# Optimization experiments

Measured on AMD Instinct MI355X. Metric: run time of the kernel, lower is better.

Reference implementation:

```python
import jax, jax.numpy as jnp
import numpy as np

B, N_SIDE, S = 64, 40, 512
N = N_SIDE * N_SIDE          # 1600 grid points (fl_feature_dims [1,40,40])
EMB = 10                     # embedding_dim
GDIM = 8                     # lie('homography').dim
WIDTH = 128
C1 = 20                      # first-layer output channels


def _embed(x, emb_dim):
    # sinusoidal embedding of each scalar coordinate: [..., D] -> [..., D*emb_dim]
    freqs = 2.0 ** jnp.arange(emb_dim // 2, dtype=x.dtype)
    ang = x[..., None] * freqs                       # [..., D, emb/2]
    e = jnp.concatenate([jnp.sin(ang), jnp.cos(ang)], axis=-1)  # [..., D, emb]
    return e.reshape(x.shape[:-1] + (x.shape[-1] * emb_dim,))


def _glorot(key, shape):
    fan_in = shape[0]
    return jax.random.normal(key, shape, dtype=jnp.float32) / np.sqrt(fan_in)


def setup_inputs() -> dict:
    key = jax.random.key(0)
    ks = jax.random.split(key, 16)
    inp = {
        'data':   jax.random.normal(ks[0], (B, N, 1), dtype=jnp.float32),
        'v0':     jax.random.normal(ks[1], (S, GDIM), dtype=jnp.float32),
        'v_last': jax.random.normal(ks[2], (S, GDIM), dtype=jnp.float32),
        # FirstLayer filter MLP: 2*EMB -> 20 -> 20 -> 1*C1
        'fl_w1': _glorot(ks[3], (2 * EMB, 20)), 'fl_b1': jnp.zeros((20,), jnp.float32),
        'fl_w2': _glorot(ks[4], (20, 20)),      'fl_b2': jnp.zeros((20,), jnp.float32),
        'fl_w3': _glorot(ks[5], (20, C1)),      'fl_b3': jnp.zeros((C1,), jnp.float32),
        # Hidden FilterMLP: EMB*GDIM=80 -> WIDTH -> C1*WIDTH
        's_w1': _glorot(ks[6], (EMB * GDIM, WIDTH)), 's_b1': jnp.zeros((WIDTH,), jnp.float32),
        's_w2': _glorot(ks[7], (WIDTH, C1 * WIDTH)), 's_b2': jnp.zeros((C1 * WIDTH,), jnp.float32),
        'fc1_w': _glorot(ks[8], (WIDTH, WIDTH)), 'fc1_b': jnp.zeros((WIDTH,), jnp.float32),
        'fc2_w': _glorot(ks[9], (WIDTH, WIDTH)), 'fc2_b': jnp.zeros((WIDTH,), jnp.float32),
        'pool_w': _glorot(ks[10], (WIDTH, 10)),  'pool_b': jnp.zeros((10,), jnp.float32),
    }
    return inp


def reference(data, v0, v_last, fl_w1, fl_b1, fl_w2, fl_b2, fl_w3, fl_b3,
              s_w1, s_b1, s_w2, s_b2, fc1_w, fc1_b, fc2_w, fc2_b, pool_w, pool_b):
    silu = jax.nn.silu
    # pixel grid in [-1,1]^2, homogeneous coords [N,3]
    lin = jnp.linspace(-1.0, 1.0, N_SIDE, dtype=data.dtype)
    xx, yy = jnp.meshgrid(lin, lin, indexing='ij')
    coords = jnp.stack([xx.ravel(), yy.ravel()], axis=-1)           # [N,2]
    xh = jnp.concatenate([coords, jnp.ones((N, 1), data.dtype)], -1)  # [N,3]
    # homography matrices: identity + small perturbation from 8 group params
    pert = jnp.concatenate([0.1 * v_last, jnp.zeros((S, 1), data.dtype)], -1).reshape(S, 3, 3)
    H = jnp.eye(3, dtype=data.dtype) + pert                          # [S,3,3]
    y = jnp.einsum('sij,nj->sni', H, xh)                             # [S,N,3]
    t = y[..., :2] / y[..., 2:3]                                     # projective action [S,N,2]
    # continuous-kernel first layer: filters generated by MLP on embedded coords
    e1 = _embed(t, EMB)                                              # [S,N,20]
    h = silu(e1 @ fl_w1 + fl_b1)
    h = silu(h @ fl_w2 + fl_b2)
    filt1 = h @ fl_w3 + fl_b3                                        # [S,N,C1]
    z = jnp.einsum('bn,sno->bso', data[:, :, 0], filt1) / N          # [B,S,C1]
    z = silu(z)
    # hidden FilterMLP on group samples v0 -> per-sample filters [S,C1,WIDTH]
    v0e = _embed(v0, EMB)                                            # [S,80]
    h2 = silu(v0e @ s_w1 + s_b1)                                     # [S,WIDTH]
    filt2 = (h2 @ s_w2 + s_b2).reshape(S, C1, WIDTH)
    # (1/S) * sum over group-sample and channel axes of broadcast product
    z = jnp.einsum('bsc,scw->bw', z, filt2) / S                      # [B,WIDTH]
    z = silu(z @ fc1_w + fc1_b) + z
    z = silu(z @ fc2_w + fc2_b) + z
    return z @ pool_w + pool_b                                       # [B,10]
```

## Files before the change

kernel.cpp:

```cpp
#include <hip/hip_runtime.h>

#define N_PTS 1600
#define NSIDE 40
#define SNUM  512
#define BNUM  64
#define C1D   20
#define WID   128

typedef _Float16 h8  __attribute__((ext_vector_type(8)));
typedef _Float16 h4  __attribute__((ext_vector_type(4)));
typedef __fp16   h2v __attribute__((ext_vector_type(2)));
typedef float    f4  __attribute__((ext_vector_type(4)));

__device__ __forceinline__ float silu_f(float x){
    return x * __builtin_amdgcn_rcpf(1.f + __expf(-x));
}
__device__ __forceinline__ void fma4(float4& a, float s, const float4 w){
    a.x += s*w.x; a.y += s*w.y; a.z += s*w.z; a.w += s*w.w;
}

__global__ __launch_bounds__(512) void kp_prep(
    const float* __restrict__ data, const float* __restrict__ v0,
    const float* __restrict__ s_w1, const float* __restrict__ s_b1,
    const float* __restrict__ s_w2,
    _Float16* __restrict__ dataA, _Float16* __restrict__ s_w2hT,
    _Float16* __restrict__ h2G, float* __restrict__ out2g)
{
    const int t = threadIdx.x, bx = blockIdx.x;
    if (bx >= 32) {
        if (bx < 112) {
            const int u  = (bx - 32) * 512 + t;
            const int n  = u >> 4, k0 = (u & 15) * 8;
            h8 v;
            #pragma unroll
            for (int j = 0; j < 8; j++) v[j] = (_Float16)s_w2[(k0 + j) * 2560 + n];
            *(h8*)(s_w2hT + n * 128 + k0) = v;
        } else if (bx < 137) {
            const int o  = (bx - 112) * 512 + t;
            const int L  = o & 63, cm = o >> 6;
            const int mt = cm & 3, ch = cm >> 2;
            const int b  = mt * 16 + (L & 15);
            const int nb = ch * 32 + (L >> 4) * 8;
            const float* src = data + b * N_PTS + nb;
            h8 v;
            #pragma unroll
            for (int j = 0; j < 8; j++) v[j] = (_Float16)src[j];
            *(h8*)(dataA + (size_t)o * 8) = v;
        } else {
            for (int v = t; v < 8192; v += 512) out2g[v] = 0.f;
        }
        return;
    }
    const int s0 = bx * 16;
    __shared__ __align__(16) _Float16 w1T[12288];
    __shared__ __align__(16) _Float16 svtA[1536];
    for (int u = t; u < 12288; u += 512) {
        const int j = u / 96, k = u - j * 96;
        w1T[u] = (_Float16)((k < 80) ? s_w1[k * 128 + j] : 0.f);
    }
    for (int u = t; u < 1536; u += 512) svtA[u] = (_Float16)0.f;
    __syncthreads();
    if (t < 128) {
        const int ss = t >> 3, d = t & 7;
        const float val = v0[(s0 + ss) * 8 + d];
        float sv, cv;
        __sincosf(val, &sv, &cv);
        #pragma unroll
        for (int k = 0; k < 5; k++) {
            svtA[ss * 96 + d * 10 + k]     = (_Float16)sv;
            svtA[ss * 96 + d * 10 + 5 + k] = (_Float16)cv;
            const float ns = 2.f * sv * cv, nc = 1.f - 2.f * sv * sv;
            sv = ns; cv = nc;
        }
    }
    __syncthreads();
    const int lane = t & 63, w = t >> 6;
    const int q = lane >> 4, l15 = lane & 15;
    const f4 zero4 = (f4)(0.f);
    f4 D = zero4;
    #pragma unroll
    for (int kc = 0; kc < 3; kc++) {
        const h8 af = *(const h8*)(svtA + l15 * 96 + kc * 32 + q * 8);
        const h8 bf = *(const h8*)(w1T + (w * 16 + l15) * 96 + kc * 32 + q * 8);
        D = __builtin_amdgcn_mfma_f32_16x16x32_f16(af, bf, D, 0, 0, 0);
    }
    const float b = s_b1[w * 16 + l15];
    #pragma unroll
    for (int r = 0; r < 4; r++)
        h2G[(s0 + q * 4 + r) * 128 + w * 16 + l15] = (_Float16)silu_f(D[r] + b);
}

__device__ __forceinline__ void embed_coord(
    int n, float hA, float hB, float hC, float h6, float h7, float h8c,
    h2v e5[5])
{
    const int i = n / NSIDE;
    const int j = n - i * NSIDE;
    const float x = -1.f + (float)i * (2.f/39.f);
    const float y = -1.f + (float)j * (2.f/39.f);
    const float yc = hA*x + hB*y + hC;
    const float y2 = h6*x + h7*y + h8c;
    const float tc = yc * __builtin_amdgcn_rcpf(y2);
    float e[10];
    float sv, cv;
    __sincosf(tc, &sv, &cv);
    #pragma unroll
    for (int k = 0; k < 5; k++) {
        e[k] = sv; e[5+k] = cv;
        const float ns = 2.f*sv*cv, nc = 1.f - 2.f*sv*sv; sv = ns; cv = nc;
    }
    #pragma unroll
    for (int k = 0; k < 5; k++)
        e5[k] = __builtin_amdgcn_cvt_pkrtz(e[2*k], e[2*k+1]);
}

#define ASTRIDE 40

__global__ __launch_bounds__(512, 8) void kaf_fused(
    const float* __restrict__ v_last,
    const float* __restrict__ w1, const float* __restrict__ b1,
    const float* __restrict__ w2, const float* __restrict__ b2,
    const float* __restrict__ w3, const float* __restrict__ b3,
    const float* __restrict__ s_b2,
    const _Float16* __restrict__ s_w2hT, const _Float16* __restrict__ h2G,
    float* __restrict__ f2g, _Float16* __restrict__ filtG)
{
    const int t  = threadIdx.x;
    const int bx = blockIdx.x;
    const int lane = t & 63, w = t >> 6;
    const int q = lane >> 4, l15 = lane & 15;
    const f4 zero4 = (f4)(0.f);

    __shared__ __align__(16) unsigned char smem[27008];

    if (bx >= 1024) {
        const int bxe = bx - 1024;
        const int mt = bxe / 10, ct = bxe - mt * 10;
        h8 af[4];
        #pragma unroll
        for (int kc = 0; kc < 4; kc++)
            af[kc] = *(const h8*)(h2G + (mt * 16 + l15) * 128 + kc * 32 + q * 8);
        #pragma unroll
        for (int i = 0; i < 2; i++) {
            const int n0 = ct * 256 + (w + 8 * i) * 16;
            f4 D = zero4;
            #pragma unroll
            for (int kc = 0; kc < 4; kc++) {
                const h8 bf = *(const h8*)(s_w2hT + (n0 + l15) * 128 + kc * 32 + q * 8);
                D = __builtin_amdgcn_mfma_f32_16x16x32_f16(af[kc], bf, D, 0, 0, 0);
            }
            const float bb = s_b2[n0 + l15];
            #pragma unroll
            for (int r = 0; r < 4; r++)
                f2g[(mt * 16 + q * 4 + r) * 2560 + n0 + l15] = D[r] + bb;
        }
        return;
    }

    const int s    = bx & 511;
    const int half = bx >> 9;
    const int nb0  = half * 800;
    const int ep   = lane >> 1;
    const int ec   = lane & 1;
    const int erow = w*16 + ep + ((ep >> 4) * 112);

    _Float16* act  = (_Float16*)smem;
    _Float16* wlds = (_Float16*)(smem + 20480);
    float*    blds = (float*)   (smem + 26624);

    {
        const float* wsrc[3] = { w1, w2, w3 };
        const float* bsrc[3] = { b1, b2, b3 };
        for (int v = t; v < 3072; v += 512) {
            const int l = v >> 10, rem = v & 1023;
            const int cout = rem >> 5, cin = rem & 31;
            float x = 0.f;
            if (cout < 20 && cin < 20) x = wsrc[l][cin * 20 + cout];
            wlds[v] = (_Float16)x;
        }
        if (t < 96) {
            const int l = t >> 5, cout = t & 31;
            blds[t] = (cout < 20) ? bsrc[l][cout] : 0.f;
        }
    }

    float Hm[9];
    #pragma unroll
    for (int k = 0; k < 9; k++) Hm[k] = (k == 0 || k == 4 || k == 8) ? 1.f : 0.f;
    #pragma unroll
    for (int k = 0; k < 8; k++) Hm[k] += 0.1f * v_last[s*8 + k];
    const float hA = ec ? Hm[3] : Hm[0];
    const float hB = ec ? Hm[4] : Hm[1];
    const float hC = ec ? Hm[5] : Hm[2];

    if (ec == 0) {
        unsigned long long* pz = (unsigned long long*)(act + erow*ASTRIDE + 20);
        pz[0] = 0ull; pz[1] = 0ull; pz[2] = 0ull;
    }

    __syncthreads();

    _Float16* fgs = filtG + (size_t)(half*512 + s) * 16000;

    for (int base = 0; base < 800; base += 256) {
        const int tn = min(256, 800 - base);

        if (erow < tn) {
            h2v e5[5];
            embed_coord(nb0 + base + erow, hA, hB, hC, Hm[6], Hm[7], Hm[8], e5);
            #pragma unroll
            for (int k = 0; k < 5; k++)
                *(h2v*)(act + erow*ASTRIDE + ec*10 + 2*k) = e5[k];
        }

        const int nmt  = tn >> 4;
        const bool hasA = w < nmt;
        const bool hasB = (w + 8) < nmt;
        const int rA = w * 16, rB = (w + 8) * 16;

        #pragma unroll
        for (int l = 0; l < 2; l++) {
            const h8 wf0 = *(const h8*)(wlds + ((l*2+0)*16 + l15) * 32 + q*8);
            const h8 wf1 = *(const h8*)(wlds + ((l*2+1)*16 + l15) * 32 + q*8);
            const float4 bD0 = *(const float4*)&blds[l*32 + q*4];
            const float4 bD1 = *(const float4*)&blds[l*32 + 16 + q*4];
            if (hasA) {
                const h8 af = *(const h8*)(act + (rA + l15)*ASTRIDE + q*8);
                const f4 D0 = __builtin_amdgcn_mfma_f32_16x16x32_f16(wf0, af, zero4, 0, 0, 0);
                const f4 D1 = __builtin_amdgcn_mfma_f32_16x16x32_f16(wf1, af, zero4, 0, 0, 0);
                h4 pv;
                pv[0] = (_Float16)silu_f(D0[0] + bD0.x);
                pv[1] = (_Float16)silu_f(D0[1] + bD0.y);
                pv[2] = (_Float16)silu_f(D0[2] + bD0.z);
                pv[3] = (_Float16)silu_f(D0[3] + bD0.w);
                *(h4*)(act + (rA + l15)*ASTRIDE + q*4) = pv;
                if (q == 0) {
                    h4 pu;
                    pu[0] = (_Float16)silu_f(D1[0] + bD1.x);
                    pu[1] = (_Float16)silu_f(D1[1] + bD1.y);
                    pu[2] = (_Float16)silu_f(D1[2] + bD1.z);
                    pu[3] = (_Float16)silu_f(D1[3] + bD1.w);
                    *(h4*)(act + (rA + l15)*ASTRIDE + 16) = pu;
                }
            }
            if (hasB) {
                const h8 af = *(const h8*)(act + (rB + l15)*ASTRIDE + q*8);
                const f4 D0 = __builtin_amdgcn_mfma_f32_16x16x32_f16(wf0, af, zero4, 0, 0, 0);
                const f4 D1 = __builtin_amdgcn_mfma_f32_16x16x32_f16(wf1, af, zero4, 0, 0, 0);
                h4 pv;
                pv[0] = (_Float16)silu_f(D0[0] + bD0.x);
                pv[1] = (_Float16)silu_f(D0[1] + bD0.y);
                pv[2] = (_Float16)silu_f(D0[2] + bD0.z);
                pv[3] = (_Float16)silu_f(D0[3] + bD0.w);
                *(h4*)(act + (rB + l15)*ASTRIDE + q*4) = pv;
                if (q == 0) {
                    h4 pu;
                    pu[0] = (_Float16)silu_f(D1[0] + bD1.x);
                    pu[1] = (_Float16)silu_f(D1[1] + bD1.y);
                    pu[2] = (_Float16)silu_f(D1[2] + bD1.z);
                    pu[3] = (_Float16)silu_f(D1[3] + bD1.w);
                    *(h4*)(act + (rB + l15)*ASTRIDE + 16) = pu;
                }
            }
        }
        {
            const h8 wf0 = *(const h8*)(wlds + (64 + l15) * 32 + q*8);
            const h8 wf1 = *(const h8*)(wlds + (80 + l15) * 32 + q*8);
            const float b20 = blds[64 + l15];
            const float b21 = blds[80 + l15];
            for (int mt = w; mt < nmt; mt += 8) {
                const int r0 = mt * 16;
                const h8 af = *(const h8*)(act + (r0 + l15)*ASTRIDE + q*8);
                f4 D0 = __builtin_amdgcn_mfma_f32_16x16x32_f16(af, wf0, zero4, 0, 0, 0);
                f4 D1 = __builtin_amdgcn_mfma_f32_16x16x32_f16(af, wf1, zero4, 0, 0, 0);
                h4 p0, p1;
                #pragma unroll
                for (int r = 0; r < 4; r++) {
                    p0[r] = (_Float16)(D0[r] + b20);
                    p1[r] = (_Float16)(D1[r] + b21);
                }
                *(h4*)(fgs + l15*800 + base + r0 + q*4) = p0;
                if (l15 < 4)
                    *(h4*)(fgs + (16 + l15)*800 + base + r0 + q*4) = p1;
            }
        }
    }
}

__global__ __launch_bounds__(256, 6) void kz_gemm(
    const _Float16* __restrict__ dataA, const _Float16* __restrict__ filtG,
    float* __restrict__ zpart)
{
    const int s    = blockIdx.x & 511;
    const int half = blockIdx.x >> 9;
    const int t    = threadIdx.x;
    const int lane = t & 63;
    const int w    = t >> 6;
    const int q    = lane >> 4;
    const int l15  = lane & 15;

    __shared__ __align__(16) float red[4 * 64 * 21];

    const _Float16* fgs = filtG + (size_t)(half*512 + s) * 16000;
    const int r1row = (l15 < 4) ? (16 + l15) : 0;

    f4 zacc[4][2];
    #pragma unroll
    for (int mt = 0; mt < 4; mt++) { zacc[mt][0] = (f4)(0.f); zacc[mt][1] = (f4)(0.f); }

    #pragma unroll 2
    for (int kc = w; kc < 25; kc += 4) {
        const h8 bf0 = *(const h8*)(fgs + l15  *800 + kc*32 + q*8);
        const h8 bf1 = *(const h8*)(fgs + r1row*800 + kc*32 + q*8);
        const int gchunk = half*25 + kc;
        #pragma unroll
        for (int mt = 0; mt < 4; mt++) {
            const h8 afz = *(const h8*)(dataA + ((size_t)(gchunk*4 + mt)*64 + lane)*8);
            zacc[mt][0] = __builtin_amdgcn_mfma_f32_16x16x32_f16(afz, bf0, zacc[mt][0], 0, 0, 0);
            zacc[mt][1] = __builtin_amdgcn_mfma_f32_16x16x32_f16(afz, bf1, zacc[mt][1], 0, 0, 0);
        }
    }

    #pragma unroll
    for (int mt = 0; mt < 4; mt++) {
        #pragma unroll
        for (int r = 0; r < 4; r++) {
            const int b = mt*16 + q*4 + r;
            red[(w*64 + b)*21 + l15] = zacc[mt][0][r];
            if (l15 < 4) red[(w*64 + b)*21 + 16 + l15] = zacc[mt][1][r];
        }
    }
    __syncthreads();
    for (int v = t; v < 1280; v += 256) {
        const int c = v >> 6, b = v & 63;
        const float sum = red[(      b)*21 + c] + red[( 64 + b)*21 + c]
                        + red[(128 + b)*21 + c] + red[(192 + b)*21 + c];
        zpart[(half*512 + s)*1280 + v] = sum;
    }
}

__global__ __launch_bounds__(256) void k2_contract(
    const float* __restrict__ zg, const float* __restrict__ f2g,
    float* __restrict__ out2g)
{
    const int blk = blockIdx.x;
    const int sg  = blk >> 2;
    const int wq  = blk & 3;
    const int s0  = sg * 4;
    const int w0  = wq * 32;
    const int t   = threadIdx.x;
    __shared__ __align__(16) float zl[4*1280];
    __shared__ __align__(16) float fl[4*20*32];
    #pragma unroll
    for (int sp = 0; sp < 4; sp++) {
        const int srow = (s0 + sp) * 1280;
        for (int r = t; r < 1280; r += 256) {
            const float a0 = zg[srow + r];
            const float a1 = zg[512*1280 + srow + r];
            zl[sp*1280 + r] = silu_f((a0 + a1) * (1.f / (float)N_PTS));
        }
        for (int u = t; u < 640; u += 256) {
            const int c = u >> 5, ww = u & 31;
            fl[sp*640 + u] = f2g[(s0 + sp)*2560 + c*128 + w0 + ww];
        }
    }
    __syncthreads();
    const int ww = t & 31, bh = t >> 5;
    float4 acc[2];
    acc[0] = make_float4(0.f, 0.f, 0.f, 0.f);
    acc[1] = make_float4(0.f, 0.f, 0.f, 0.f);
    #pragma unroll 4
    for (int sc = 0; sc < 80; sc++) {
        const float f = fl[sc * 32 + ww];
        const float4* zz = (const float4*)&zl[sc * 64 + bh * 8];
        fma4(acc[0], f, zz[0]);
        fma4(acc[1], f, zz[1]);
    }
    const float* af = (const float*)acc;
    #pragma unroll
    for (int idx = 0; idx < 8; idx++) {
        const int b = bh * 8 + idx;
        atomicAdd(&out2g[b * 128 + w0 + ww], af[idx]);
    }
}

__global__ __launch_bounds__(128) void k3_tail(
    const float* __restrict__ out2g,
    const float* __restrict__ fc1w, const float* __restrict__ fc1b,
    const float* __restrict__ fc2w, const float* __restrict__ fc2b,
    const float* __restrict__ pw,   const float* __restrict__ pb,
    float* __restrict__ out)
{
    const int b = blockIdx.x, t = threadIdx.x;
    __shared__ float zb[128], r1[128], r2[128];
    zb[t] = out2g[b * 128 + t] * (1.f / (float)SNUM);
    __syncthreads();
    float a = fc1b[t];
    #pragma unroll 8
    for (int i = 0; i < 128; i++) a += zb[i] * fc1w[i * 128 + t];
    r1[t] = silu_f(a) + zb[t];
    __syncthreads();
    a = fc2b[t];
    #pragma unroll 8
    for (int i = 0; i < 128; i++) a += r1[i] * fc2w[i * 128 + t];
    r2[t] = silu_f(a) + r1[t];
    __syncthreads();
    if (t < 10) {
        float o = pb[t];
        #pragma unroll 8
        for (int i = 0; i < 128; i++) o += r2[i] * pw[i * 10 + t];
        out[b * 10 + t] = o;
    }
}

extern "C" void kernel_launch(void* const* d_in, const int* in_sizes, int n_in,
                              void* d_out, int out_size, void* d_ws, size_t ws_size,
                              hipStream_t stream) {
    const float* data   = (const float*)d_in[0];
    const float* v0     = (const float*)d_in[1];
    const float* v_last = (const float*)d_in[2];
    const float* fl_w1  = (const float*)d_in[3];
    const float* fl_b1  = (const float*)d_in[4];
    const float* fl_w2  = (const float*)d_in[5];
    const float* fl_b2  = (const float*)d_in[6];
    const float* fl_w3  = (const float*)d_in[7];
    const float* fl_b3  = (const float*)d_in[8];
    const float* s_w1   = (const float*)d_in[9];
    const float* s_b1   = (const float*)d_in[10];
    const float* s_w2   = (const float*)d_in[11];
    const float* s_b2   = (const float*)d_in[12];
    const float* fc1_w  = (const float*)d_in[13];
    const float* fc1_b  = (const float*)d_in[14];
    const float* fc2_w  = (const float*)d_in[15];
    const float* fc2_b  = (const float*)d_in[16];
    const float* pool_w = (const float*)d_in[17];
    const float* pool_b = (const float*)d_in[18];
    float* out = (float*)d_out;

    float* ws        = (float*)d_ws;
    _Float16* dataA  = (_Float16*)ws;
    float* zpart  = ws    + 51200;
    float* f2g    = zpart + 1310720;
    float* out2g  = f2g   + 1310720;
    _Float16* s_w2hT = (_Float16*)(out2g + 8192);
    _Float16* h2G    = (_Float16*)(out2g + 8192 + 163840);
    _Float16* filtG  = (_Float16*)(out2g + 8192 + 163840 + 32768);

    kp_prep    <<<138, 512, 0, stream>>>(data, v0, s_w1, s_b1, s_w2,
                                         dataA, s_w2hT, h2G, out2g);
    kaf_fused  <<<1344, 512, 0, stream>>>(v_last,
                                          fl_w1, fl_b1, fl_w2, fl_b2, fl_w3, fl_b3,
                                          s_b2, s_w2hT, h2G, f2g, filtG);
    kz_gemm    <<<1024, 256, 0, stream>>>(dataA, filtG, zpart);
    k2_contract<<<512, 256, 0, stream>>>(zpart, f2g, out2g);
    k3_tail    <<<64, 128, 0, stream>>>(out2g, fc1_w, fc1_b, fc2_w, fc2_b,
                                        pool_w, pool_b, out);
}
```

Baseline: 164.2 us.

## Fuse filter generation with data contraction, keeping filters in LDS

```diff
diff --git a/kernel.cpp b/kernel.cpp
--- a/kernel.cpp
+++ b/kernel.cpp
@@ -116,14 +116,15 @@
 
 #define ASTRIDE 40
 
-__global__ __launch_bounds__(512, 8) void kaf_fused(
+__global__ __launch_bounds__(512, 8) void kfz_fused(
     const float* __restrict__ v_last,
     const float* __restrict__ w1, const float* __restrict__ b1,
     const float* __restrict__ w2, const float* __restrict__ b2,
     const float* __restrict__ w3, const float* __restrict__ b3,
     const float* __restrict__ s_b2,
     const _Float16* __restrict__ s_w2hT, const _Float16* __restrict__ h2G,
-    float* __restrict__ f2g, _Float16* __restrict__ filtG)
+    const _Float16* __restrict__ dataA,
+    float* __restrict__ f2g, float* __restrict__ zpart)
 {
     const int t  = threadIdx.x;
     const int bx = blockIdx.x;
@@ -131,7 +132,7 @@
     const int q = lane >> 4, l15 = lane & 15;
     const f4 zero4 = (f4)(0.f);
 
-    __shared__ __align__(16) unsigned char smem[27008];
+    __shared__ __align__(16) unsigned char smem[37632];
 
     if (bx >= 1024) {
         const int bxe = bx - 1024;
@@ -163,10 +164,14 @@
     const int ep   = lane >> 1;
     const int ec   = lane & 1;
     const int erow = w*16 + ep + ((ep >> 4) * 112);
-
-    _Float16* act  = (_Float16*)smem;
-    _Float16* wlds = (_Float16*)(smem + 20480);
-    float*    blds = (float*)   (smem + 26624);
+    const int mtbase = (w & 1) * 2;
+    const int kcs    = w >> 1;
+
+    _Float16* act   = (_Float16*)smem;
+    _Float16* filtB = (_Float16*)(smem + 20480);
+    _Float16* wlds  = (_Float16*)(smem + 31040);
+    float*    blds  = (float*)   (smem + 37184);
+    float*    red   = (float*)smem;
 
     {
         const float* wsrc[3] = { w1, w2, w3 };
@@ -198,9 +203,11 @@
         pz[0] = 0ull; pz[1] = 0ull; pz[2] = 0ull;
     }
 
-    __syncthreads();
-
-    _Float16* fgs = filtG + (size_t)(half*512 + s) * 16000;
+    f4 zacc[2][2];
+    #pragma unroll
+    for (int mi = 0; mi < 2; mi++) { zacc[mi][0] = zero4; zacc[mi][1] = zero4; }
+
+    __syncthreads();
 
     for (int base = 0; base < 800; base += 256) {
         const int tn = min(256, 800 - base);
@@ -279,62 +286,51 @@
                     p0[r] = (_Float16)(D0[r] + b20);
                     p1[r] = (_Float16)(D1[r] + b21);
                 }
-                *(h4*)(fgs + l15*800 + base + r0 + q*4) = p0;
+                *(h4*)(filtB + l15*264 + r0 + q*4) = p0;
                 if (l15 < 4)
-                    *(h4*)(fgs + (16 + l15)*800 + base + r0 + q*4) = p1;
+                    *(h4*)(filtB + (16 + l15)*264 + r0 + q*4) = p1;
             }
         }
-    }
-}
-
-__global__ __launch_bounds__(256, 6) void kz_gemm(
-    const _Float16* __restrict__ dataA, const _Float16* __restrict__ filtG,
-    float* __restrict__ zpart)
-{
-    const int s    = blockIdx.x & 511;
-    const int half = blockIdx.x >> 9;
-    const int t    = threadIdx.x;
-    const int lane = t & 63;
-    const int w    = t >> 6;
-    const int q    = lane >> 4;
-    const int l15  = lane & 15;
-
-    __shared__ __align__(16) float red[4 * 64 * 21];
-
-    const _Float16* fgs = filtG + (size_t)(half*512 + s) * 16000;
-    const int r1row = (l15 < 4) ? (16 + l15) : 0;
-
-    f4 zacc[4][2];
-    #pragma unroll
-    for (int mt = 0; mt < 4; mt++) { zacc[mt][0] = (f4)(0.f); zacc[mt][1] = (f4)(0.f); }
-
-    #pragma unroll 2
-    for (int kc = w; kc < 25; kc += 4) {
-        const h8 bf0 = *(const h8*)(fgs + l15  *800 + kc*32 + q*8);
-        const h8 bf1 = *(const h8*)(fgs + r1row*800 + kc*32 + q*8);
-        const int gchunk = half*25 + kc;
-        #pragma unroll
-        for (int mt = 0; mt < 4; mt++) {
-            const h8 afz = *(const h8*)(dataA + ((size_t)(gchunk*4 + mt)*64 + lane)*8);
-            zacc[mt][0] = __builtin_amdgcn_mfma_f32_16x16x32_f16(afz, bf0, zacc[mt][0], 0, 0, 0);
-            zacc[mt][1] = __builtin_amdgcn_mfma_f32_16x16x32_f16(afz, bf1, zacc[mt][1], 0, 0, 0);
-        }
-    }
-
-    #pragma unroll
-    for (int mt = 0; mt < 4; mt++) {
+        __syncthreads();
+
+        const int nkc = tn >> 5;
+        const int r1row = (l15 < 4) ? (16 + l15) : 0;
+        #pragma unroll
+        for (int kk = 0; kk < 2; kk++) {
+            const int kc = kcs + kk*4;
+            if (kc < nkc) {
+                const int gchunk = ((nb0 + base) >> 5) + kc;
+                const h8 bf0 = *(const h8*)(filtB + l15  *264 + kc*32 + q*8);
+                const h8 bf1 = *(const h8*)(filtB + r1row*264 + kc*32 + q*8);
+                #pragma unroll
+                for (int mi = 0; mi < 2; mi++) {
+                    const int mt = mtbase + mi;
+                    const h8 afz = *(const h8*)(dataA + ((size_t)(gchunk*4 + mt)*64 + lane)*8);
+                    zacc[mi][0] = __builtin_amdgcn_mfma_f32_16x16x32_f16(afz, bf0, zacc[mi][0], 0, 0, 0);
+                    zacc[mi][1] = __builtin_amdgcn_mfma_f32_16x16x32_f16(afz, bf1, zacc[mi][1], 0, 0, 0);
+                }
+            }
+        }
+        __syncthreads();
+    }
+
+    #pragma unroll
+    for (int mi = 0; mi < 2; mi++) {
         #pragma unroll
         for (int r = 0; r < 4; r++) {
-            const int b = mt*16 + q*4 + r;
-            red[(w*64 + b)*21 + l15] = zacc[mt][0][r];
-            if (l15 < 4) red[(w*64 + b)*21 + 16 + l15] = zacc[mt][1][r];
-        }
-    }
-    __syncthreads();
-    for (int v = t; v < 1280; v += 256) {
+            const int bl = mi*16 + q*4 + r;
+            red[(w*32 + bl)*21 + l15] = zacc[mi][0][r];
+            if (l15 < 4) red[(w*32 + bl)*21 + 16 + l15] = zacc[mi][1][r];
+        }
+    }
+    __syncthreads();
+    for (int v = t; v < 1280; v += 512) {
         const int c = v >> 6, b = v & 63;
-        const float sum = red[(      b)*21 + c] + red[( 64 + b)*21 + c]
-                        + red[(128 + b)*21 + c] + red[(192 + b)*21 + c];
+        const int mts = b >> 5, bl = b & 31;
+        const float sum = red[((mts    )*32 + bl)*21 + c]
+                        + red[((mts + 2)*32 + bl)*21 + c]
+                        + red[((mts + 4)*32 + bl)*21 + c]
+                        + red[((mts + 6)*32 + bl)*21 + c];
         zpart[(half*512 + s)*1280 + v] = sum;
     }
 }
@@ -444,14 +440,12 @@
     float* out2g  = f2g   + 1310720;
     _Float16* s_w2hT = (_Float16*)(out2g + 8192);
     _Float16* h2G    = (_Float16*)(out2g + 8192 + 163840);
-    _Float16* filtG  = (_Float16*)(out2g + 8192 + 163840 + 32768);
 
     kp_prep    <<<138, 512, 0, stream>>>(data, v0, s_w1, s_b1, s_w2,
                                          dataA, s_w2hT, h2G, out2g);
-    kaf_fused  <<<1344, 512, 0, stream>>>(v_last,
+    kfz_fused  <<<1344, 512, 0, stream>>>(v_last,
                                           fl_w1, fl_b1, fl_w2, fl_b2, fl_w3, fl_b3,
-                                          s_b2, s_w2hT, h2G, f2g, filtG);
-    kz_gemm    <<<1024, 256, 0, stream>>>(dataA, filtG, zpart);
+                                          s_b2, s_w2hT, h2G, dataA, f2g, zpart);
     k2_contract<<<512, 256, 0, stream>>>(zpart, f2g, out2g);
     k3_tail    <<<64, 128, 0, stream>>>(out2g, fc1_w, fc1_b, fc2_w, fc2_b,
                                         pool_w, pool_b, out);
```

New measurement: 167.7 us. +2.2%, slower.

## Replace MFMA tile-based filter MLP with per-thread scalar FP32 MLP

Applied to the files above, without the earlier changes.

```diff
diff --git a/kernel.cpp b/kernel.cpp
--- a/kernel.cpp
+++ b/kernel.cpp
@@ -9,7 +9,6 @@
 
 typedef _Float16 h8  __attribute__((ext_vector_type(8)));
 typedef _Float16 h4  __attribute__((ext_vector_type(4)));
-typedef __fp16   h2v __attribute__((ext_vector_type(2)));
 typedef float    f4  __attribute__((ext_vector_type(4)));
 
 __device__ __forceinline__ float silu_f(float x){
@@ -90,33 +89,7 @@
         h2G[(s0 + q * 4 + r) * 128 + w * 16 + l15] = (_Float16)silu_f(D[r] + b);
 }
 
-__device__ __forceinline__ void embed_coord(
-    int n, float hA, float hB, float hC, float h6, float h7, float h8c,
-    h2v e5[5])
-{
-    const int i = n / NSIDE;
-    const int j = n - i * NSIDE;
-    const float x = -1.f + (float)i * (2.f/39.f);
-    const float y = -1.f + (float)j * (2.f/39.f);
-    const float yc = hA*x + hB*y + hC;
-    const float y2 = h6*x + h7*y + h8c;
-    const float tc = yc * __builtin_amdgcn_rcpf(y2);
-    float e[10];
-    float sv, cv;
-    __sincosf(tc, &sv, &cv);
-    #pragma unroll
-    for (int k = 0; k < 5; k++) {
-        e[k] = sv; e[5+k] = cv;
-        const float ns = 2.f*sv*cv, nc = 1.f - 2.f*sv*sv; sv = ns; cv = nc;
-    }
-    #pragma unroll
-    for (int k = 0; k < 5; k++)
-        e5[k] = __builtin_amdgcn_cvt_pkrtz(e[2*k], e[2*k+1]);
-}
-
-#define ASTRIDE 40
-
-__global__ __launch_bounds__(512, 8) void kaf_fused(
+__global__ __launch_bounds__(512) void kfv_filt(
     const float* __restrict__ v_last,
     const float* __restrict__ w1, const float* __restrict__ b1,
     const float* __restrict__ w2, const float* __restrict__ b2,
@@ -127,14 +100,12 @@
 {
     const int t  = threadIdx.x;
     const int bx = blockIdx.x;
-    const int lane = t & 63, w = t >> 6;
-    const int q = lane >> 4, l15 = lane & 15;
-    const f4 zero4 = (f4)(0.f);
-
-    __shared__ __align__(16) unsigned char smem[27008];
-
-    if (bx >= 1024) {
-        const int bxe = bx - 1024;
+
+    if (bx >= 1600) {
+        const int lane = t & 63, w = t >> 6;
+        const int q = lane >> 4, l15 = lane & 15;
+        const f4 zero4 = (f4)(0.f);
+        const int bxe = bx - 1600;
         const int mt = bxe / 10, ct = bxe - mt * 10;
         h8 af[4];
         #pragma unroll
@@ -157,134 +128,81 @@
         return;
     }
 
-    const int s    = bx & 511;
-    const int half = bx >> 9;
-    const int nb0  = half * 800;
-    const int ep   = lane >> 1;
-    const int ec   = lane & 1;
-    const int erow = w*16 + ep + ((ep >> 4) * 112);
-
-    _Float16* act  = (_Float16*)smem;
-    _Float16* wlds = (_Float16*)(smem + 20480);
-    float*    blds = (float*)   (smem + 26624);
-
+    const int tid  = bx * 512 + t;
+    const int s    = tid / 1600;
+    const int p    = tid - s * 1600;
+    const int half = (p >= 800) ? 1 : 0;
+    const int row  = p - half * 800;
+
+    float Hm[9];
+    #pragma unroll
+    for (int k = 0; k < 9; k++) Hm[k] = (k == 0 || k == 4 || k == 8) ? 1.f : 0.f;
+    #pragma unroll
+    for (int k = 0; k < 8; k++) Hm[k] += 0.1f * v_last[s * 8 + k];
+
+    const int gi = p / NSIDE;
+    const int gj = p - gi * NSIDE;
+    const float x = -1.f + (float)gi * (2.f / 39.f);
+    const float y = -1.f + (float)gj * (2.f / 39.f);
+    const float den = Hm[6] * x + Hm[7] * y + Hm[8];
+    const float inv = __builtin_amdgcn_rcpf(den);
+    const float t0 = (Hm[0] * x + Hm[1] * y + Hm[2]) * inv;
+    const float t1 = (Hm[3] * x + Hm[4] * y + Hm[5]) * inv;
+
+    float e[20];
     {
-        const float* wsrc[3] = { w1, w2, w3 };
-        const float* bsrc[3] = { b1, b2, b3 };
-        for (int v = t; v < 3072; v += 512) {
-            const int l = v >> 10, rem = v & 1023;
-            const int cout = rem >> 5, cin = rem & 31;
-            float x = 0.f;
-            if (cout < 20 && cin < 20) x = wsrc[l][cin * 20 + cout];
-            wlds[v] = (_Float16)x;
-        }
-        if (t < 96) {
-            const int l = t >> 5, cout = t & 31;
-            blds[t] = (cout < 20) ? bsrc[l][cout] : 0.f;
-        }
-    }
-
-    float Hm[9];
-    #pragma unroll
-    for (int k = 0; k < 9; k++) Hm[k] = (k == 0 || k == 4 || k == 8) ? 1.f : 0.f;
-    #pragma unroll
-    for (int k = 0; k < 8; k++) Hm[k] += 0.1f * v_last[s*8 + k];
-    const float hA = ec ? Hm[3] : Hm[0];
-    const float hB = ec ? Hm[4] : Hm[1];
-    const float hC = ec ? Hm[5] : Hm[2];
-
-    if (ec == 0) {
-        unsigned long long* pz = (unsigned long long*)(act + erow*ASTRIDE + 20);
-        pz[0] = 0ull; pz[1] = 0ull; pz[2] = 0ull;
-    }
-
-    __syncthreads();
-
-    _Float16* fgs = filtG + (size_t)(half*512 + s) * 16000;
-
-    for (int base = 0; base < 800; base += 256) {
-        const int tn = min(256, 800 - base);
-
-        if (erow < tn) {
-            h2v e5[5];
-            embed_coord(nb0 + base + erow, hA, hB, hC, Hm[6], Hm[7], Hm[8], e5);
-            #pragma unroll
-            for (int k = 0; k < 5; k++)
-                *(h2v*)(act + erow*ASTRIDE + ec*10 + 2*k) = e5[k];
-        }
-
-        const int nmt  = tn >> 4;
-        const bool hasA = w < nmt;
-        const bool hasB = (w + 8) < nmt;
-        const int rA = w * 16, rB = (w + 8) * 16;
-
-        #pragma unroll
-        for (int l = 0; l < 2; l++) {
-            const h8 wf0 = *(const h8*)(wlds + ((l*2+0)*16 + l15) * 32 + q*8);
-            const h8 wf1 = *(const h8*)(wlds + ((l*2+1)*16 + l15) * 32 + q*8);
-            const float4 bD0 = *(const float4*)&blds[l*32 + q*4];
-            const float4 bD1 = *(const float4*)&blds[l*32 + 16 + q*4];
-            if (hasA) {
-                const h8 af = *(const h8*)(act + (rA + l15)*ASTRIDE + q*8);
-                const f4 D0 = __builtin_amdgcn_mfma_f32_16x16x32_f16(wf0, af, zero4, 0, 0, 0);
-                const f4 D1 = __builtin_amdgcn_mfma_f32_16x16x32_f16(wf1, af, zero4, 0, 0, 0);
-                h4 pv;
-                pv[0] = (_Float16)silu_f(D0[0] + bD0.x);
-                pv[1] = (_Float16)silu_f(D0[1] + bD0.y);
-                pv[2] = (_Float16)silu_f(D0[2] + bD0.z);
-                pv[3] = (_Float16)silu_f(D0[3] + bD0.w);
-                *(h4*)(act + (rA + l15)*ASTRIDE + q*4) = pv;
-                if (q == 0) {
-                    h4 pu;
-                    pu[0] = (_Float16)silu_f(D1[0] + bD1.x);
-                    pu[1] = (_Float16)silu_f(D1[1] + bD1.y);
-                    pu[2] = (_Float16)silu_f(D1[2] + bD1.z);
-                    pu[3] = (_Float16)silu_f(D1[3] + bD1.w);
-                    *(h4*)(act + (rA + l15)*ASTRIDE + 16) = pu;
-                }
-            }
-            if (hasB) {
-                const h8 af = *(const h8*)(act + (rB + l15)*ASTRIDE + q*8);
-                const f4 D0 = __builtin_amdgcn_mfma_f32_16x16x32_f16(wf0, af, zero4, 0, 0, 0);
-                const f4 D1 = __builtin_amdgcn_mfma_f32_16x16x32_f16(wf1, af, zero4, 0, 0, 0);
-                h4 pv;
-                pv[0] = (_Float16)silu_f(D0[0] + bD0.x);
-                pv[1] = (_Float16)silu_f(D0[1] + bD0.y);
-                pv[2] = (_Float16)silu_f(D0[2] + bD0.z);
-                pv[3] = (_Float16)silu_f(D0[3] + bD0.w);
-                *(h4*)(act + (rB + l15)*ASTRIDE + q*4) = pv;
-                if (q == 0) {
-                    h4 pu;
-                    pu[0] = (_Float16)silu_f(D1[0] + bD1.x);
-                    pu[1] = (_Float16)silu_f(D1[1] + bD1.y);
-                    pu[2] = (_Float16)silu_f(D1[2] + bD1.z);
-                    pu[3] = (_Float16)silu_f(D1[3] + bD1.w);
-                    *(h4*)(act + (rB + l15)*ASTRIDE + 16) = pu;
-                }
-            }
-        }
-        {
-            const h8 wf0 = *(const h8*)(wlds + (64 + l15) * 32 + q*8);
-            const h8 wf1 = *(const h8*)(wlds + (80 + l15) * 32 + q*8);
-            const float b20 = blds[64 + l15];
-            const float b21 = blds[80 + l15];
-            for (int mt = w; mt < nmt; mt += 8) {
-                const int r0 = mt * 16;
-                const h8 af = *(const h8*)(act + (r0 + l15)*ASTRIDE + q*8);
-                f4 D0 = __builtin_amdgcn_mfma_f32_16x16x32_f16(af, wf0, zero4, 0, 0, 0);
-                f4 D1 = __builtin_amdgcn_mfma_f32_16x16x32_f16(af, wf1, zero4, 0, 0, 0);
-                h4 p0, p1;
-                #pragma unroll
-                for (int r = 0; r < 4; r++) {
-                    p0[r] = (_Float16)(D0[r] + b20);
-                    p1[r] = (_Float16)(D1[r] + b21);
-                }
-                *(h4*)(fgs + l15*800 + base + r0 + q*4) = p0;
-                if (l15 < 4)
-                    *(h4*)(fgs + (16 + l15)*800 + base + r0 + q*4) = p1;
-            }
-        }
-    }
+        float sv, cv;
+        __sincosf(t0, &sv, &cv);
+        #pragma unroll
+        for (int k = 0; k < 5; k++) {
+            e[k] = sv; e[5 + k] = cv;
+            const float ns = 2.f * sv * cv, nc = 1.f - 2.f * sv * sv;
+            sv = ns; cv = nc;
+        }
+        __sincosf(t1, &sv, &cv);
+        #pragma unroll
+        for (int k = 0; k < 5; k++) {
+            e[10 + k] = sv; e[15 + k] = cv;
+            const float ns = 2.f * sv * cv, nc = 1.f - 2.f * sv * sv;
+            sv = ns; cv = nc;
+        }
+    }
+
+    float h[20], hn[20];
+    #pragma unroll
+    for (int j = 0; j < 20; j++) hn[j] = b1[j];
+    #pragma unroll
+    for (int k = 0; k < 20; k++) {
+        const float ek = e[k];
+        #pragma unroll
+        for (int j = 0; j < 20; j++) hn[j] += ek * w1[k * 20 + j];
+    }
+    #pragma unroll
+    for (int j = 0; j < 20; j++) h[j] = silu_f(hn[j]);
+
+    #pragma unroll
+    for (int j = 0; j < 20; j++) hn[j] = b2[j];
+    #pragma unroll
+    for (int k = 0; k < 20; k++) {
+        const float hk = h[k];
+        #pragma unroll
+        for (int j = 0; j < 20; j++) hn[j] += hk * w2[k * 20 + j];
+    }
+    #pragma unroll
+    for (int j = 0; j < 20; j++) h[j] = silu_f(hn[j]);
+
+    #pragma unroll
+    for (int j = 0; j < 20; j++) hn[j] = b3[j];
+    #pragma unroll
+    for (int k = 0; k < 20; k++) {
+        const float hk = h[k];
+        #pragma unroll
+        for (int j = 0; j < 20; j++) hn[j] += hk * w3[k * 20 + j];
+    }
+    _Float16* fgs = filtG + (size_t)(half * 512 + s) * 16000;
+    #pragma unroll
+    for (int c = 0; c < 20; c++)
+        fgs[c * 800 + row] = (_Float16)hn[c];
 }
 
 __global__ __launch_bounds__(256, 6) void kz_gemm(
@@ -448,7 +366,7 @@
 
     kp_prep    <<<138, 512, 0, stream>>>(data, v0, s_w1, s_b1, s_w2,
                                          dataA, s_w2hT, h2G, out2g);
-    kaf_fused  <<<1344, 512, 0, stream>>>(v_last,
+    kfv_filt   <<<1920, 512, 0, stream>>>(v_last,
                                           fl_w1, fl_b1, fl_w2, fl_b2, fl_w3, fl_b3,
                                           s_b2, s_w2hT, h2G, f2g, filtG);
     kz_gemm    <<<1024, 256, 0, stream>>>(dataA, filtG, zpart);
```

New measurement: 182.9 us. 1.11x slower.
